# Kernel optimization log

Hardware: AMD Instinct MI355X
Metric: run time of the kernel (lower is better)

Reference implementation:

```python
import jax, jax.numpy as jnp
import numpy as np

K = 9  # kernel_size (kNN neighbors, includes self since loop=True)


def _knn_edges(x_f, batch, k):
    # x_f: [N, C]. Full pairwise squared distances, masked across batch groups.
    N = x_f.shape[0]
    sq = jnp.sum(x_f * x_f, axis=1)
    d2 = sq[:, None] - 2.0 * (x_f @ x_f.T) + sq[None, :]          # [N, N]
    same = batch[:, None] == batch[None, :]
    d2 = jnp.where(same, d2, jnp.inf)
    neg_d, idx = jax.lax.top_k(-d2, k)                             # k nearest per query row
    valid = jnp.isfinite(neg_d)                                    # guard tiny groups (<k nodes)
    src = idx.reshape(-1)                                          # neighbor -> source
    tgt = jnp.repeat(jnp.arange(N), k)                             # query    -> target
    return src, tgt, valid.reshape(-1)


def _cheb_conv(x_f, src, tgt, valid, W0, W1, bias):
    # ChebConv, K=2, normalization='sym', lambda_max=2.0:
    #   out = x @ W0 + (L_hat x) @ W1 + b,  L_hat = -D^{-1/2} A D^{-1/2} (diag 0)
    N = x_f.shape[0]
    w = jnp.where(valid & (src != tgt), 1.0, 0.0)                  # remove_self_loops
    deg = jax.ops.segment_sum(w, src, num_segments=N)
    dis = jnp.where(deg > 0, jax.lax.rsqrt(jnp.maximum(deg, 1e-30)), 0.0)
    norm = -dis[src] * w * dis[tgt]                                # off-diag of scaled Laplacian
    Tx1 = jax.ops.segment_sum(norm[:, None] * x_f[src], tgt, num_segments=N)
    return x_f @ W0 + Tx1 @ W1 + bias


def setup_inputs() -> dict:
    key = jax.random.key(0)
    k1, k2, k3, k4 = jax.random.split(key, 4)
    B, C, H, W = 8, 192, 32, 32
    Cout = 192
    return {
        "x": jax.random.normal(k1, (B, C, H, W), dtype=jnp.float32),
        "W0": jax.random.normal(k2, (C, Cout), dtype=jnp.float32) * (1.0 / np.sqrt(C)),
        "W1": jax.random.normal(k3, (C, Cout), dtype=jnp.float32) * (1.0 / np.sqrt(C)),
        "bias": jax.random.normal(k4, (Cout,), dtype=jnp.float32) * 0.01,
    }


def reference(x, W0, W1, bias):
    B, C, H, W = x.shape
    N = B * H * W
    x_f = jnp.transpose(x, (0, 2, 3, 1)).reshape(N, C)             # flat_nodes: [B*H*W, C]
    # torch.linspace(0, B, steps=N, dtype=int64) -> truncated float linspace
    batch = jnp.linspace(0.0, float(B), N).astype(jnp.int32)
    src, tgt, valid = _knn_edges(x_f, batch, K)
    return _cheb_conv(x_f, src, tgt, valid, W0, W1, bias)
```

## Files before the change

kernel.cpp:

```cpp
#include <hip/hip_runtime.h>
#include <math.h>

#define NN 8192
#define CF 192
#define KNN 9
#define NSPL 8

typedef __bf16 v8bf __attribute__((ext_vector_type(8)));
typedef float f32x16 __attribute__((ext_vector_type(16)));
typedef float f32x4 __attribute__((ext_vector_type(4)));

__device__ __forceinline__ int group_start(int g) {
    int s = (8191 * g + 7) >> 3;
    return s > 8192 ? 8192 : s;
}

__device__ __forceinline__ float disf(int d) {
    return d > 0 ? 1.0f / sqrtf((float)d) : 0.0f;
}

__device__ __forceinline__ unsigned short f2bf(float f) {
    unsigned u = __float_as_uint(f);
    unsigned r = (u + 0x7FFFu + ((u >> 16) & 1u)) >> 16;
    return (unsigned short)r;
}
__device__ __forceinline__ float bf2f(unsigned short h) {
    return __uint_as_float(((unsigned)h) << 16);
}

__global__ __launch_bounds__(256) void transpose_kernel(
    const float* __restrict__ x, unsigned short* __restrict__ xh,
    unsigned short* __restrict__ xl, float* __restrict__ sq,
    int* __restrict__ deg)
{
    __shared__ float tile[32][65];
    int b = blockIdx.x, ht = blockIdx.y;
    int hw0 = ht * 64;
    int tid = threadIdx.x;
    if (tid < 64) deg[(b * 16 + ht) * 64 + tid] = 0;

    float sacc[8];
#pragma unroll
    for (int p = 0; p < 8; ++p) sacc[p] = 0.0f;

    for (int ct = 0; ct < 6; ++ct) {
        int c0 = ct * 32;
        __syncthreads();
#pragma unroll
        for (int p = 0; p < 8; ++p) {
            int c  = p * 4 + (tid >> 6);
            int hw = tid & 63;
            tile[c][hw] = x[(size_t)b * 196608 + (size_t)(c0 + c) * 1024 + hw0 + hw];
        }
        __syncthreads();
#pragma unroll
        for (int p = 0; p < 8; ++p) {
            int hw = p * 8 + (tid >> 5);
            int cc = tid & 31;
            float v = tile[cc][hw];
            size_t o = (size_t)(b * 1024 + hw0 + hw) * CF + c0 + cc;
            unsigned short h = f2bf(v);
            xh[o] = h;
            xl[o] = f2bf(v - bf2f(h));
            sacc[p] = fmaf(v, v, sacc[p]);
        }
    }
#pragma unroll
    for (int p = 0; p < 8; ++p) {
        float s = sacc[p];
#pragma unroll
        for (int off = 16; off > 0; off >>= 1) s += __shfl_xor(s, off, 32);
        if ((tid & 31) == 0)
            sq[(size_t)(b * 1024 + hw0 + p * 8 + (tid >> 5))] = s;
    }
}

__global__ __launch_bounds__(256, 2) void knn_kernel(
    const unsigned short* __restrict__ xh, const unsigned short* __restrict__ xl,
    const float* __restrict__ sq,
    float* __restrict__ pk_d, int* __restrict__ pk_i)
{
    int bid = blockIdx.x;
    int g = bid >> 7;
    int rem = bid & 127;
    int qb = rem >> 3;
    int split = rem & 7;
    int gs = group_start(g);
    int gsize = group_start(g + 1) - gs;
    int q0 = qb * 64;
    int nq = gsize - q0; if (nq > 64) nq = 64;
    if (nq <= 0) return;
    int c0 = split * 128;
    int ncc = gsize - c0; if (ncc > 128) ncc = 128;

    int tid = threadIdx.x;

    float td[KNN]; int ti[KNN];
#pragma unroll
    for (int j = 0; j < KNN; ++j) { td[j] = __builtin_inff(); ti[j] = -1; }

    if (ncc <= 0) {
        if (tid < nq) {
            int q = gs + q0 + tid;
            size_t base = ((size_t)q * NSPL + split) * KNN;
#pragma unroll
            for (int j = 0; j < KNN; ++j) { pk_d[base + j] = td[j]; pk_i[base + j] = ti[j]; }
        }
        return;
    }

    __shared__ __align__(16) char smem[28192];
    unsigned short (*Ah)[24] = (unsigned short(*)[24])smem;
    unsigned short (*Al)[24] = (unsigned short(*)[24])(smem + 3072);
    unsigned short (*Bh)[24] = (unsigned short(*)[24])(smem + 6144);
    unsigned short (*Bl)[24] = (unsigned short(*)[24])(smem + 12288);
    float (*ld)[KNN][65] = (float(*)[KNN][65])smem;
    int   (*li)[KNN][65] = (int(*)[KNN][65])(smem + 9360);
    float (*Ds)[37] = (float(*)[37])(smem + 18720);
    __shared__ float sqc_s[128];
    __shared__ float sqq_s[64];

    int lane = tid & 63, w = tid >> 6;
    int arow = (w & 1) * 32 + (lane & 31);
    int k8 = (lane >> 5) * 8;
    int brow0 = (w >> 1) * 64 + (lane & 31);

    if (tid < 64) {
        int qo = q0 + tid; if (qo > gsize - 1) qo = gsize - 1;
        sqq_s[tid] = sq[gs + qo];
    }
    if (tid < 128) {
        sqc_s[tid] = (tid < ncc) ? sq[gs + c0 + tid] : __builtin_inff();
    }

    int a_hl = tid >> 7, a_r = (tid >> 1) & 63, a_half = tid & 1;
    int a_qo = q0 + a_r; if (a_qo > gsize - 1) a_qo = gsize - 1;
    const unsigned short* a_src = (a_hl ? xl : xh)
        + (size_t)(gs + a_qo) * CF + a_half * 8;
    unsigned short* a_dst = (a_hl ? (unsigned short*)Al : (unsigned short*)Ah)
        + a_r * 24 + a_half * 8;

    f32x16 acc[2];
#pragma unroll
    for (int t = 0; t < 2; ++t)
#pragma unroll
        for (int r = 0; r < 16; ++r) acc[t][r] = 0.0f;

    for (int kb = 0; kb < 12; ++kb) {
        __syncthreads();
        *(uint4*)a_dst = *(const uint4*)(a_src + kb * 16);
#pragma unroll
        for (int p = 0; p < 2; ++p) {
            int t = tid + 256 * p;
            int hl = t >> 8, r = (t >> 1) & 127, half = t & 1;
            int co = c0 + r; if (co > gsize - 1) co = gsize - 1;
            const unsigned short* src = (hl ? xl : xh)
                + (size_t)(gs + co) * CF + kb * 16 + half * 8;
            unsigned short* dst = (hl ? (unsigned short*)Bl : (unsigned short*)Bh)
                + r * 24 + half * 8;
            *(uint4*)dst = *(const uint4*)src;
        }
        __syncthreads();
        v8bf a_hi = *(const v8bf*)&Ah[arow][k8];
        v8bf a_lo = *(const v8bf*)&Al[arow][k8];
#pragma unroll
        for (int t = 0; t < 2; ++t) {
            v8bf b_hi = *(const v8bf*)&Bh[brow0 + t * 32][k8];
            v8bf b_lo = *(const v8bf*)&Bl[brow0 + t * 32][k8];
            acc[t] = __builtin_amdgcn_mfma_f32_32x32x16_bf16(a_hi, b_hi, acc[t], 0, 0, 0);
            acc[t] = __builtin_amdgcn_mfma_f32_32x32x16_bf16(a_lo, b_hi, acc[t], 0, 0, 0);
            acc[t] = __builtin_amdgcn_mfma_f32_32x32x16_bf16(a_hi, b_lo, acc[t], 0, 0, 0);
        }
    }

#pragma unroll
    for (int qt = 0; qt < 4; ++qt) {
        __syncthreads();
        if ((w >> 1) == (qt >> 1)) {
#pragma unroll
            for (int r = 0; r < 16; ++r) {
                int row = (w & 1) * 32 + (r & 3) + 8 * (r >> 2) + 4 * (lane >> 5);
                Ds[row][lane & 31] = acc[qt & 1][r];
            }
        }
        __syncthreads();
        {
            int q = tid & 63, ch = tid >> 6;
            float sqq = sqq_s[q];
            float pd[KNN]; int pi[KNN];
#pragma unroll
            for (int j = 0; j < KNN; ++j) { pd[j] = __builtin_inff(); pi[j] = -1; }
#pragma unroll
            for (int j8 = 0; j8 < 8; ++j8) {
                int c = ch * 8 + j8;
                float d = (sqq - 2.0f * Ds[q][c]) + sqc_s[qt * 32 + c];
                if (d < pd[KNN - 1]) {
                    pd[KNN - 1] = d; pi[KNN - 1] = gs + c0 + qt * 32 + c;
#pragma unroll
                    for (int j = KNN - 1; j > 0; --j) {
                        if (pd[j] < pd[j - 1]) {
                            float tf = pd[j]; pd[j] = pd[j - 1]; pd[j - 1] = tf;
                            int tn = pi[j]; pi[j] = pi[j - 1]; pi[j - 1] = tn;
                        }
                    }
                }
            }
#pragma unroll
            for (int j = 0; j < KNN; ++j) { ld[ch][j][q] = pd[j]; li[ch][j][q] = pi[j]; }
        }
        __syncthreads();
        if (tid < 64) {
            for (int ch = 0; ch < 4; ++ch) {
#pragma unroll
                for (int j0 = 0; j0 < KNN; ++j0) {
                    float d = ld[ch][j0][tid];
                    if (!(d < td[KNN - 1])) break;
                    int id = li[ch][j0][tid];
                    td[KNN - 1] = d; ti[KNN - 1] = id;
#pragma unroll
                    for (int j = KNN - 1; j > 0; --j) {
                        if (td[j] < td[j - 1]) {
                            float tf = td[j]; td[j] = td[j - 1]; td[j - 1] = tf;
                            int tn = ti[j]; ti[j] = ti[j - 1]; ti[j - 1] = tn;
                        }
                    }
                }
            }
        }
    }

    if (tid < nq) {
        int q = gs + q0 + tid;
        size_t base = ((size_t)q * NSPL + split) * KNN;
#pragma unroll
        for (int j = 0; j < KNN; ++j) { pk_d[base + j] = td[j]; pk_i[base + j] = ti[j]; }
    }
}

__global__ __launch_bounds__(64) void merge_kernel(
    const float* __restrict__ pk_d, const int* __restrict__ pk_i,
    int* __restrict__ edges, int* __restrict__ deg,
    const float* __restrict__ W0, const float* __restrict__ W1,
    unsigned short* __restrict__ wt)
{
    __shared__ float wtile[32][33];
    int tid = threadIdx.x;
    if (blockIdx.x >= 128) {
        int wid = blockIdx.x - 128;
        int mat = wid / 36, rem2 = wid % 36;
        int k0 = (rem2 / 6) * 32, n0 = (rem2 % 6) * 32;
        const float* W = mat ? W1 : W0;
#pragma unroll
        for (int p = 0; p < 4; ++p) {
            int idx = p * 64 + tid;
            int k = idx >> 3, n4 = (idx & 7) * 4;
            *(float4*)&wtile[k][n4] =
                *(const float4*)(W + (size_t)(k0 + k) * CF + n0 + n4);
        }
        __syncthreads();
#pragma unroll
        for (int p = 0; p < 4; ++p) {
            int idx = p * 64 + tid;
            int n = idx >> 3, k4 = (idx & 7) * 4;
            ushort4 h;
            h.x = f2bf(wtile[k4 + 0][n]); h.y = f2bf(wtile[k4 + 1][n]);
            h.z = f2bf(wtile[k4 + 2][n]); h.w = f2bf(wtile[k4 + 3][n]);
            *(ushort4*)(wt + (size_t)mat * 36864 + (size_t)(n0 + n) * CF + k0 + k4) = h;
        }
        return;
    }
    int q = blockIdx.x * 64 + tid;
    float td[KNN]; int ti[KNN];
#pragma unroll
    for (int j = 0; j < KNN; ++j) { td[j] = __builtin_inff(); ti[j] = -1; }
    for (int s = 0; s < NSPL; ++s) {
        size_t base = ((size_t)q * NSPL + s) * KNN;
#pragma unroll
        for (int j0 = 0; j0 < KNN; ++j0) {
            float d = pk_d[base + j0];
            if (!(d < td[KNN - 1])) break;
            int id = pk_i[base + j0];
            td[KNN - 1] = d; ti[KNN - 1] = id;
#pragma unroll
            for (int j = KNN - 1; j > 0; --j) {
                if (td[j] < td[j - 1]) {
                    float tf = td[j]; td[j] = td[j - 1]; td[j - 1] = tf;
                    int tn = ti[j]; ti[j] = ti[j - 1]; ti[j - 1] = tn;
                }
            }
        }
    }
#pragma unroll
    for (int j = 0; j < KNN; ++j) {
        int id = ti[j];
        edges[q * KNN + j] = id;
        if (id >= 0 && id != q) atomicAdd(&deg[id], 1);
    }
}

__global__ __launch_bounds__(256, 2) void out_kernel(
    const unsigned short* __restrict__ xh, const unsigned short* __restrict__ wt,
    const int* __restrict__ edges, const int* __restrict__ deg,
    const float* __restrict__ bias, float* __restrict__ out)
{
    __shared__ unsigned short A0s[16][200];
    __shared__ unsigned short A1s[16][200];
    __shared__ unsigned short Wts[2][CF][32];
    __shared__ float coef_s[16][KNN];
    __shared__ int   nb_s[16][KNN];

    int r0 = blockIdx.x * 16;
    int tid = threadIdx.x;

    for (int t = tid; t < 384; t += 256) {
        int i = t / 24, c8 = (t % 24) * 8;
        *(uint4*)&A0s[i][c8] = *(const uint4*)(xh + (size_t)(r0 + i) * CF + c8);
    }
    if (tid < 16 * KNN) {
        int i = tid / KNN, j = tid % KNN;
        int q = r0 + i;
        int id = edges[q * KNN + j];
        float cf = 0.0f; int s = q;
        if (id >= 0 && id != q) { cf = -disf(deg[id]) * disf(deg[q]); s = id; }
        coef_s[i][j] = cf; nb_s[i][j] = s;
    }
    __syncthreads();
    for (int e = tid; e < 16 * CF / 2; e += 256) {
        int i = e / 96, c2 = (e % 96) * 2;
        float a0 = 0.0f, a1 = 0.0f;
#pragma unroll
        for (int t = 0; t < KNN; ++t) {
            const unsigned short* row = xh + (size_t)nb_s[i][t] * CF + c2;
            float cf = coef_s[i][t];
            a0 = fmaf(cf, bf2f(row[0]), a0);
            a1 = fmaf(cf, bf2f(row[1]), a1);
        }
        ushort2 h; h.x = f2bf(a0); h.y = f2bf(a1);
        *(ushort2*)&A1s[i][c2] = h;
    }

    int lane = tid & 63, w = tid >> 6;
    int m = lane & 15;
    int kq = (lane >> 4) * 8;
    f32x4 acc[3];
#pragma unroll
    for (int t = 0; t < 3; ++t)
#pragma unroll
        for (int r = 0; r < 4; ++r) acc[t][r] = 0.0f;

    for (int kt = 0; kt < 6; ++kt) {
        __syncthreads();
#pragma unroll
        for (int p = 0; p < 6; ++p) {
            int f = p * 256 + tid;
            int mat = f / 768, n = (f % 768) / 4, k16 = (f % 4) * 8;
            *(uint4*)&Wts[mat][n][k16] =
                *(const uint4*)(wt + (size_t)mat * 36864 + (size_t)n * CF + kt * 32 + k16);
        }
        __syncthreads();
        v8bf a0 = *(const v8bf*)&A0s[m][kt * 32 + kq];
        v8bf a1 = *(const v8bf*)&A1s[m][kt * 32 + kq];
#pragma unroll
        for (int t3 = 0; t3 < 3; ++t3) {
            int n0 = w * 48 + t3 * 16;
            v8bf w0 = *(const v8bf*)&Wts[0][n0 + m][kq];
            v8bf w1 = *(const v8bf*)&Wts[1][n0 + m][kq];
            acc[t3] = __builtin_amdgcn_mfma_f32_16x16x32_bf16(a0, w0, acc[t3], 0, 0, 0);
            acc[t3] = __builtin_amdgcn_mfma_f32_16x16x32_bf16(a1, w1, acc[t3], 0, 0, 0);
        }
    }

    int col = lane & 15, rb = (lane >> 4) * 4;
#pragma unroll
    for (int t3 = 0; t3 < 3; ++t3) {
        int n0 = w * 48 + t3 * 16;
        float bv = bias[n0 + col];
#pragma unroll
        for (int r = 0; r < 4; ++r)
            out[(size_t)(r0 + rb + r) * CF + n0 + col] = acc[t3][r] + bv;
    }
}

extern "C" void kernel_launch(void* const* d_in, const int* in_sizes, int n_in,
                              void* d_out, int out_size, void* d_ws, size_t ws_size,
                              hipStream_t stream)
{
    const float* x    = (const float*)d_in[0];
    const float* W0   = (const float*)d_in[1];
    const float* W1   = (const float*)d_in[2];
    const float* bias = (const float*)d_in[3];
    float* out = (float*)d_out;

    char* ws = (char*)d_ws;
    unsigned short* xh = (unsigned short*)ws; ws += (size_t)NN * CF * 2;
    unsigned short* xl = (unsigned short*)ws; ws += (size_t)NN * CF * 2;
    float* sq    = (float*)ws;  ws += (size_t)NN * 4;
    int*   deg   = (int*)ws;    ws += (size_t)NN * 4;
    int*   edges = (int*)ws;    ws += (size_t)NN * KNN * 4;

    unsigned short* wt = xl;

    float* pk_d = out;
    int*   pk_i = (int*)(out + (size_t)NN * NSPL * KNN);

    hipLaunchKernelGGL(transpose_kernel, dim3(8, 16), dim3(256), 0, stream,
                       x, xh, xl, sq, deg);
    hipLaunchKernelGGL(knn_kernel, dim3(1152), dim3(256), 0, stream,
                       xh, xl, sq, pk_d, pk_i);
    hipLaunchKernelGGL(merge_kernel, dim3(200), dim3(64), 0, stream,
                       pk_d, pk_i, edges, deg, W0, W1, wt);
    hipLaunchKernelGGL(out_kernel, dim3(512), dim3(256), 0, stream,
                       xh, wt, edges, deg, bias, out);
}
```

Before: 151.3 us.

## Prefetch kNN tiles into registers, defer top-k merge, vectorize gathers and partial loads

The kNN kernel now loads the next k-slice of the A and B tiles into registers while MFMAs run on the current one. Each thread keeps its running top-k across all four column sub-tiles and merges into the block's lists once at the end, instead of a shared-memory merge with extra barriers per sub-tile. Partial top-k records are padded to 12 entries so the merge kernel can read them with float4/int4 loads. The neighbour aggregation in out_kernel now gathers 8 bf16 values per 16-byte load instead of scalar loads. These changes add register pressure, and the padded stride writes into the output buffer used as scratch.

```diff
diff --git a/kernel.cpp b/kernel.cpp
--- a/kernel.cpp
+++ b/kernel.cpp
@@ -5,6 +5,7 @@
 #define CF 192
 #define KNN 9
 #define NSPL 8
+#define PKS 12
 
 typedef __bf16 v8bf __attribute__((ext_vector_type(8)));
 typedef float f32x16 __attribute__((ext_vector_type(16)));
@@ -95,16 +96,12 @@
 
     int tid = threadIdx.x;
 
-    float td[KNN]; int ti[KNN];
-#pragma unroll
-    for (int j = 0; j < KNN; ++j) { td[j] = __builtin_inff(); ti[j] = -1; }
-
     if (ncc <= 0) {
         if (tid < nq) {
             int q = gs + q0 + tid;
-            size_t base = ((size_t)q * NSPL + split) * KNN;
-#pragma unroll
-            for (int j = 0; j < KNN; ++j) { pk_d[base + j] = td[j]; pk_i[base + j] = ti[j]; }
+            size_t base = ((size_t)q * NSPL + split) * PKS;
+#pragma unroll
+            for (int j = 0; j < KNN; ++j) { pk_d[base + j] = __builtin_inff(); pk_i[base + j] = -1; }
         }
         return;
     }
@@ -130,7 +127,7 @@
         sqq_s[tid] = sq[gs + qo];
     }
     if (tid < 128) {
-        sqc_s[tid] = (tid < ncc) ? sq[gs + c0 + tid] : __builtin_inff();
+        sqc_s[tid] = (tid < 128 && tid < ncc) ? sq[gs + c0 + tid] : __builtin_inff();
     }
 
     int a_hl = tid >> 7, a_r = (tid >> 1) & 63, a_half = tid & 1;
@@ -140,27 +137,34 @@
     unsigned short* a_dst = (a_hl ? (unsigned short*)Al : (unsigned short*)Ah)
         + a_r * 24 + a_half * 8;
 
+    int b_r = (tid >> 1) & 127, b_half = tid & 1;
+    int b_co = c0 + b_r; if (b_co > gsize - 1) b_co = gsize - 1;
+    const unsigned short* b_src0 = xh + (size_t)(gs + b_co) * CF + b_half * 8;
+    const unsigned short* b_src1 = xl + (size_t)(gs + b_co) * CF + b_half * 8;
+    unsigned short* b_dst0 = (unsigned short*)Bh + b_r * 24 + b_half * 8;
+    unsigned short* b_dst1 = (unsigned short*)Bl + b_r * 24 + b_half * 8;
+
     f32x16 acc[2];
 #pragma unroll
     for (int t = 0; t < 2; ++t)
 #pragma unroll
         for (int r = 0; r < 16; ++r) acc[t][r] = 0.0f;
 
+    uint4 rA  = *(const uint4*)a_src;
+    uint4 rB0 = *(const uint4*)b_src0;
+    uint4 rB1 = *(const uint4*)b_src1;
+
     for (int kb = 0; kb < 12; ++kb) {
         __syncthreads();
-        *(uint4*)a_dst = *(const uint4*)(a_src + kb * 16);
-#pragma unroll
-        for (int p = 0; p < 2; ++p) {
-            int t = tid + 256 * p;
-            int hl = t >> 8, r = (t >> 1) & 127, half = t & 1;
-            int co = c0 + r; if (co > gsize - 1) co = gsize - 1;
-            const unsigned short* src = (hl ? xl : xh)
-                + (size_t)(gs + co) * CF + kb * 16 + half * 8;
-            unsigned short* dst = (hl ? (unsigned short*)Bl : (unsigned short*)Bh)
-                + r * 24 + half * 8;
-            *(uint4*)dst = *(const uint4*)src;
-        }
-        __syncthreads();
+        *(uint4*)a_dst  = rA;
+        *(uint4*)b_dst0 = rB0;
+        *(uint4*)b_dst1 = rB1;
+        __syncthreads();
+        if (kb < 11) {
+            rA  = *(const uint4*)(a_src  + (kb + 1) * 16);
+            rB0 = *(const uint4*)(b_src0 + (kb + 1) * 16);
+            rB1 = *(const uint4*)(b_src1 + (kb + 1) * 16);
+        }
         v8bf a_hi = *(const v8bf*)&Ah[arow][k8];
         v8bf a_lo = *(const v8bf*)&Al[arow][k8];
 #pragma unroll
@@ -173,6 +177,12 @@
         }
     }
 
+    int sq_ = tid & 63, sch = tid >> 6;
+    float sqqv = sqq_s[sq_];
+    float pd[KNN]; int pi[KNN];
+#pragma unroll
+    for (int j = 0; j < KNN; ++j) { pd[j] = __builtin_inff(); pi[j] = -1; }
+
 #pragma unroll
     for (int qt = 0; qt < 4; ++qt) {
         __syncthreads();
@@ -184,56 +194,66 @@
             }
         }
         __syncthreads();
-        {
-            int q = tid & 63, ch = tid >> 6;
-            float sqq = sqq_s[q];
-            float pd[KNN]; int pi[KNN];
-#pragma unroll
-            for (int j = 0; j < KNN; ++j) { pd[j] = __builtin_inff(); pi[j] = -1; }
-#pragma unroll
-            for (int j8 = 0; j8 < 8; ++j8) {
-                int c = ch * 8 + j8;
-                float d = (sqq - 2.0f * Ds[q][c]) + sqc_s[qt * 32 + c];
-                if (d < pd[KNN - 1]) {
-                    pd[KNN - 1] = d; pi[KNN - 1] = gs + c0 + qt * 32 + c;
-#pragma unroll
-                    for (int j = KNN - 1; j > 0; --j) {
-                        if (pd[j] < pd[j - 1]) {
-                            float tf = pd[j]; pd[j] = pd[j - 1]; pd[j - 1] = tf;
-                            int tn = pi[j]; pi[j] = pi[j - 1]; pi[j - 1] = tn;
-                        }
+        float dv[8], cv[8];
+#pragma unroll
+        for (int j8 = 0; j8 < 8; ++j8) {
+            dv[j8] = Ds[sq_][sch * 8 + j8];
+            cv[j8] = sqc_s[qt * 32 + sch * 8 + j8];
+        }
+#pragma unroll
+        for (int j8 = 0; j8 < 8; ++j8) {
+            float d = (sqqv - 2.0f * dv[j8]) + cv[j8];
+            if (d < pd[KNN - 1]) {
+                pd[KNN - 1] = d; pi[KNN - 1] = gs + c0 + qt * 32 + sch * 8 + j8;
+#pragma unroll
+                for (int j = KNN - 1; j > 0; --j) {
+                    if (pd[j] < pd[j - 1]) {
+                        float tf = pd[j]; pd[j] = pd[j - 1]; pd[j - 1] = tf;
+                        int tn = pi[j]; pi[j] = pi[j - 1]; pi[j - 1] = tn;
                     }
                 }
             }
-#pragma unroll
-            for (int j = 0; j < KNN; ++j) { ld[ch][j][q] = pd[j]; li[ch][j][q] = pi[j]; }
-        }
-        __syncthreads();
-        if (tid < 64) {
-            for (int ch = 0; ch < 4; ++ch) {
-#pragma unroll
-                for (int j0 = 0; j0 < KNN; ++j0) {
-                    float d = ld[ch][j0][tid];
-                    if (!(d < td[KNN - 1])) break;
-                    int id = li[ch][j0][tid];
-                    td[KNN - 1] = d; ti[KNN - 1] = id;
-#pragma unroll
-                    for (int j = KNN - 1; j > 0; --j) {
-                        if (td[j] < td[j - 1]) {
-                            float tf = td[j]; td[j] = td[j - 1]; td[j - 1] = tf;
-                            int tn = ti[j]; ti[j] = ti[j - 1]; ti[j - 1] = tn;
-                        }
+        }
+    }
+
+#pragma unroll
+    for (int j = 0; j < KNN; ++j) { ld[sch][j][sq_] = pd[j]; li[sch][j][sq_] = pi[j]; }
+    __syncthreads();
+
+    if (tid < 64) {
+        float dL[4][KNN]; int iL[4][KNN];
+#pragma unroll
+        for (int ch = 0; ch < 4; ++ch)
+#pragma unroll
+            for (int j = 0; j < KNN; ++j) {
+                dL[ch][j] = ld[ch][j][tid];
+                iL[ch][j] = li[ch][j][tid];
+            }
+        float td[KNN]; int ti[KNN];
+#pragma unroll
+        for (int j = 0; j < KNN; ++j) { td[j] = __builtin_inff(); ti[j] = -1; }
+#pragma unroll
+        for (int ch = 0; ch < 4; ++ch) {
+#pragma unroll
+            for (int j0 = 0; j0 < KNN; ++j0) {
+                float d = dL[ch][j0];
+                if (!(d < td[KNN - 1])) break;
+                td[KNN - 1] = d; ti[KNN - 1] = iL[ch][j0];
+#pragma unroll
+                for (int j = KNN - 1; j > 0; --j) {
+                    if (td[j] < td[j - 1]) {
+                        float tf = td[j]; td[j] = td[j - 1]; td[j - 1] = tf;
+                        int tn = ti[j]; ti[j] = ti[j - 1]; ti[j - 1] = tn;
                     }
                 }
             }
         }
-    }
-
-    if (tid < nq) {
-        int q = gs + q0 + tid;
-        size_t base = ((size_t)q * NSPL + split) * KNN;
-#pragma unroll
-        for (int j = 0; j < KNN; ++j) { pk_d[base + j] = td[j]; pk_i[base + j] = ti[j]; }
+        if (tid < nq) {
+            int q = gs + q0 + tid;
+            size_t base = ((size_t)q * NSPL + split) * PKS;
+#pragma unroll
+            for (int j = 0; j < KNN; ++j) { pk_d[base + j] = td[j]; pk_i[base + j] = ti[j]; }
+        }
     }
 }
 
@@ -273,19 +293,38 @@
     float td[KNN]; int ti[KNN];
 #pragma unroll
     for (int j = 0; j < KNN; ++j) { td[j] = __builtin_inff(); ti[j] = -1; }
-    for (int s = 0; s < NSPL; ++s) {
-        size_t base = ((size_t)q * NSPL + s) * KNN;
-#pragma unroll
-        for (int j0 = 0; j0 < KNN; ++j0) {
-            float d = pk_d[base + j0];
-            if (!(d < td[KNN - 1])) break;
-            int id = pk_i[base + j0];
-            td[KNN - 1] = d; ti[KNN - 1] = id;
-#pragma unroll
-            for (int j = KNN - 1; j > 0; --j) {
-                if (td[j] < td[j - 1]) {
-                    float tf = td[j]; td[j] = td[j - 1]; td[j - 1] = tf;
-                    int tn = ti[j]; ti[j] = ti[j - 1]; ti[j - 1] = tn;
+#pragma unroll
+    for (int sb = 0; sb < 2; ++sb) {
+        float sd[4][KNN]; int si[4][KNN];
+#pragma unroll
+        for (int s2 = 0; s2 < 4; ++s2) {
+            int s = sb * 4 + s2;
+            const float* pd = pk_d + ((size_t)q * NSPL + s) * PKS;
+            const int*   pp = pk_i + ((size_t)q * NSPL + s) * PKS;
+            float4 d0 = *(const float4*)pd;
+            float4 d1 = *(const float4*)(pd + 4);
+            sd[s2][0] = d0.x; sd[s2][1] = d0.y; sd[s2][2] = d0.z; sd[s2][3] = d0.w;
+            sd[s2][4] = d1.x; sd[s2][5] = d1.y; sd[s2][6] = d1.z; sd[s2][7] = d1.w;
+            sd[s2][8] = pd[8];
+            int4 i0 = *(const int4*)pp;
+            int4 i1 = *(const int4*)(pp + 4);
+            si[s2][0] = i0.x; si[s2][1] = i0.y; si[s2][2] = i0.z; si[s2][3] = i0.w;
+            si[s2][4] = i1.x; si[s2][5] = i1.y; si[s2][6] = i1.z; si[s2][7] = i1.w;
+            si[s2][8] = pp[8];
+        }
+#pragma unroll
+        for (int s2 = 0; s2 < 4; ++s2) {
+#pragma unroll
+            for (int j0 = 0; j0 < KNN; ++j0) {
+                float d = sd[s2][j0];
+                if (!(d < td[KNN - 1])) break;
+                td[KNN - 1] = d; ti[KNN - 1] = si[s2][j0];
+#pragma unroll
+                for (int j = KNN - 1; j > 0; --j) {
+                    if (td[j] < td[j - 1]) {
+                        float tf = td[j]; td[j] = td[j - 1]; td[j - 1] = tf;
+                        int tn = ti[j]; ti[j] = ti[j - 1]; ti[j - 1] = tn;
+                    }
                 }
             }
         }
@@ -303,8 +342,8 @@
     const int* __restrict__ edges, const int* __restrict__ deg,
     const float* __restrict__ bias, float* __restrict__ out)
 {
-    __shared__ unsigned short A0s[16][200];
-    __shared__ unsigned short A1s[16][200];
+    __shared__ __align__(16) unsigned short A0s[16][200];
+    __shared__ __align__(16) unsigned short A1s[16][200];
     __shared__ unsigned short Wts[2][CF][32];
     __shared__ float coef_s[16][KNN];
     __shared__ int   nb_s[16][KNN];
@@ -325,18 +364,25 @@
         coef_s[i][j] = cf; nb_s[i][j] = s;
     }
     __syncthreads();
-    for (int e = tid; e < 16 * CF / 2; e += 256) {
-        int i = e / 96, c2 = (e % 96) * 2;
-        float a0 = 0.0f, a1 = 0.0f;
+    for (int e = tid; e < 16 * CF / 8; e += 256) {
+        int i = e / 24, c8 = (e % 24) * 8;
+        float a[8];
+#pragma unroll
+        for (int j = 0; j < 8; ++j) a[j] = 0.0f;
 #pragma unroll
         for (int t = 0; t < KNN; ++t) {
-            const unsigned short* row = xh + (size_t)nb_s[i][t] * CF + c2;
             float cf = coef_s[i][t];
-            a0 = fmaf(cf, bf2f(row[0]), a0);
-            a1 = fmaf(cf, bf2f(row[1]), a1);
-        }
-        ushort2 h; h.x = f2bf(a0); h.y = f2bf(a1);
-        *(ushort2*)&A1s[i][c2] = h;
+            uint4 v = *(const uint4*)(xh + (size_t)nb_s[i][t] * CF + c8);
+            const unsigned short* pv = (const unsigned short*)&v;
+#pragma unroll
+            for (int j = 0; j < 8; ++j) a[j] = fmaf(cf, bf2f(pv[j]), a[j]);
+        }
+        uint4 hv;
+        hv.x = (unsigned)f2bf(a[0]) | ((unsigned)f2bf(a[1]) << 16);
+        hv.y = (unsigned)f2bf(a[2]) | ((unsigned)f2bf(a[3]) << 16);
+        hv.z = (unsigned)f2bf(a[4]) | ((unsigned)f2bf(a[5]) << 16);
+        hv.w = (unsigned)f2bf(a[6]) | ((unsigned)f2bf(a[7]) << 16);
+        *(uint4*)&A1s[i][c8] = hv;
     }
 
     int lane = tid & 63, w = tid >> 6;
@@ -401,7 +447,7 @@
     unsigned short* wt = xl;
 
     float* pk_d = out;
-    int*   pk_i = (int*)(out + (size_t)NN * NSPL * KNN);
+    int*   pk_i = (int*)(out + (size_t)NN * NSPL * PKS);
 
     hipLaunchKernelGGL(transpose_kernel, dim3(8, 16), dim3(256), 0, stream,
                        x, xh, xl, sq, deg);
```

After: 131.5 us. 13.1% less time.
